# Kernel optimization log

Measured on AMD Instinct MI355X. Metric: run time of the kernel, lower is better.

Reference implementation:

```python
import jax, jax.numpy as jnp
import numpy as np

EMBED_DIM = 768
N_HEADS = 12
HEAD_DIM = EMBED_DIM // N_HEADS


def setup_inputs() -> dict:
    key = jax.random.key(0)
    ks = jax.random.split(key, 5)
    s = 1.0 / np.sqrt(EMBED_DIM)
    x = jax.random.normal(ks[0], (8, 1024, EMBED_DIM), dtype=jnp.float32)
    w_qkv = jax.random.normal(ks[1], (EMBED_DIM, 3 * EMBED_DIM), dtype=jnp.float32) * s
    b_qkv = jnp.zeros((3 * EMBED_DIM,), dtype=jnp.float32)
    w_proj = jax.random.normal(ks[2], (EMBED_DIM, EMBED_DIM), dtype=jnp.float32) * s
    b_proj = jnp.zeros((EMBED_DIM,), dtype=jnp.float32)
    return {"x": x, "w_qkv": w_qkv, "b_qkv": b_qkv, "w_proj": w_proj, "b_proj": b_proj}


def reference(x, w_qkv, b_qkv, w_proj, b_proj):
    B, S, D = x.shape
    H, Hd = N_HEADS, HEAD_DIM
    qkv = x @ w_qkv + b_qkv                      # [B,S,3D]
    qkv = qkv.reshape(B, S, 3, H, Hd).transpose(2, 0, 3, 1, 4)  # [3,B,H,S,Hd]
    q, k, v = qkv[0], qkv[1], qkv[2]
    scale = Hd ** -0.5
    attn = jnp.einsum('bhqd,bhkd->bhqk', q, k) * scale  # [B,H,S,S]
    attn = jax.nn.softmax(attn, axis=-1)
    out = jnp.einsum('bhqk,bhkd->bhqd', attn, v)        # [B,H,S,Hd]
    out = out.transpose(0, 2, 1, 3).reshape(B, S, D)
    return out @ w_proj + b_proj
```

## Files before the change

kernel.cpp:

```cpp
#include <hip/hip_runtime.h>
#include <stdint.h>

typedef unsigned short ushort_t;
typedef __bf16 bf16x8 __attribute__((ext_vector_type(8)));
typedef float floatx4 __attribute__((ext_vector_type(4)));
typedef float floatx16 __attribute__((ext_vector_type(16)));
typedef unsigned int uintx4 __attribute__((ext_vector_type(4)));

#define B_   8
#define S_   1024
#define D_   768
#define H_   12
#define M_   (B_ * S_)
#define N3_  (3 * D_)
#define QK_  1536
#define QSCALE 0.18033688f

static __device__ __forceinline__ void gl_lds16(const void* g, void* l) {
  __builtin_amdgcn_global_load_lds((const __attribute__((address_space(1))) void*)g,
                                   (__attribute__((address_space(3))) void*)l,
                                   16, 0, 0);
}

static __device__ __forceinline__ ushort_t f2bf(float f) {
  __bf16 h = (__bf16)f;
  return __builtin_bit_cast(unsigned short, h);
}

static __device__ __forceinline__ void store_out(ushort_t* p, float v) { *p = f2bf(v); }
static __device__ __forceinline__ void store_out(float* p, float v) { *p = v; }

static __device__ __forceinline__ unsigned cvt_pk_bf16(float lo, float hi) {
  unsigned d;
  asm("v_cvt_pk_bf16_f32 %0, %1, %2" : "=v"(d) : "v"(lo), "v"(hi));
  return d;
}
static __device__ __forceinline__ void plane32_swap(unsigned& a, unsigned& b) {
  asm volatile("v_permlane32_swap_b32 %0, %1" : "+v"(a), "+v"(b));
}

static __device__ __forceinline__ void transpose_tile(const float* __restrict__ W,
                                                      ushort_t* __restrict__ Wt,
                                                      int K, int N, int bx, int by,
                                                      int t) {
  __shared__ float tile[32][33];
  const int n0 = bx * 32, k0 = by * 32;
  const int tx = t & 31, ty = t >> 5;
#pragma unroll
  for (int i = 0; i < 4; ++i)
    tile[ty + i * 8][tx] = W[(size_t)(k0 + ty + i * 8) * N + n0 + tx];
  __syncthreads();
#pragma unroll
  for (int i = 0; i < 4; ++i)
    Wt[(size_t)(n0 + ty + i * 8) * K + k0 + tx] = f2bf(tile[tx][ty + i * 8]);
}

__global__ __launch_bounds__(256) void prep_kernel(const float* __restrict__ x,
                                                   ushort_t* __restrict__ xb,
                                                   const float* __restrict__ w_qkv,
                                                   ushort_t* __restrict__ wqkvt,
                                                   const float* __restrict__ w_proj,
                                                   ushort_t* __restrict__ wprojt) {
  const int gb = blockIdx.x, t = threadIdx.x;
  if (gb < 6144) {
    const int i = (gb * 256 + t) * 4;
    const float4 v = *(const float4*)(x + i);
    ushort4 o4;
    o4.x = f2bf(v.x); o4.y = f2bf(v.y); o4.z = f2bf(v.z); o4.w = f2bf(v.w);
    *(ushort4*)(xb + i) = o4;
  } else if (gb < 6144 + 1728) {
    const int lb = gb - 6144;
    transpose_tile(w_qkv, wqkvt, D_, N3_, lb % 72, lb / 72, t);
  } else {
    const int lb = gb - 6144 - 1728;
    transpose_tile(w_proj, wprojt, D_, D_, lb % 24, lb / 24, t);
  }
}

template <typename OutT, bool SPLITV>
__global__ __launch_bounds__(256) void gemm_bt_bias(const ushort_t* __restrict__ A,
                                                    const ushort_t* __restrict__ Bt,
                                                    const float* __restrict__ bias,
                                                    OutT* __restrict__ C, int CN,
                                                    ushort_t* __restrict__ vt) {
  __shared__ __align__(16) ushort_t As[128 * 32];
  __shared__ __align__(16) ushort_t Bs[128 * 32];
  const int t = threadIdx.x;
  const int wave = t >> 6, lane = t & 63;
  const int quad = lane >> 4, l15 = lane & 15;
  const int wm = wave >> 1, wn = wave & 1;
  const int m0 = blockIdx.y * 128, n0 = blockIdx.x * 128;

  const int scol  = ((lane & 3) ^ ((lane >> 3) & 3)) * 8;
  const int slotq = (quad ^ ((l15 >> 1) & 3)) * 8;

  floatx4 acc[4][4];
#pragma unroll
  for (int i = 0; i < 4; ++i)
#pragma unroll
    for (int j = 0; j < 4; ++j) acc[i][j] = (floatx4)0.0f;

  for (int k0 = 0; k0 < 768; k0 += 32) {
    if (k0) __syncthreads();
#pragma unroll
    for (int c = 0; c < 2; ++c) {
      const int i0 = c * 256 + wave * 64;
      const int i = i0 + lane;
      const int row = i >> 2;
      gl_lds16(A + (size_t)(m0 + row) * 768 + k0 + scol, As + i0 * 8);
      gl_lds16(Bt + (size_t)(n0 + row) * 768 + k0 + scol, Bs + i0 * 8);
    }
    __syncthreads();

    bf16x8 af[4], bfr[4];
#pragma unroll
    for (int mi = 0; mi < 4; ++mi)
      af[mi] = *(const bf16x8*)(As + (wm * 64 + mi * 16 + l15) * 32 + slotq);
#pragma unroll
    for (int ni = 0; ni < 4; ++ni)
      bfr[ni] = *(const bf16x8*)(Bs + (wn * 64 + ni * 16 + l15) * 32 + slotq);
#pragma unroll
    for (int mi = 0; mi < 4; ++mi)
#pragma unroll
      for (int ni = 0; ni < 4; ++ni)
        acc[mi][ni] = __builtin_amdgcn_mfma_f32_16x16x32_bf16(af[mi], bfr[ni], acc[mi][ni], 0, 0, 0);
  }

#pragma unroll
  for (int ni = 0; ni < 4; ++ni) {
    const int colb = n0 + wn * 64 + ni * 16;
    const int col = colb + l15;
    const float bb = bias[col];
    if (SPLITV && colb >= 1536) {
      const int hh = (colb - 1536) >> 6;
      const int d  = ((colb - 1536) & 63) + l15;
      const int bh = (m0 >> 10) * H_ + hh;
      ushort_t* vrow = vt + ((size_t)bh * 64 + d) * 1024 +
                       (m0 & 1023) + wm * 64 + quad * 4;
#pragma unroll
      for (int mi = 0; mi < 4; ++mi) {
        ushort4 pk;
        pk.x = f2bf(acc[mi][ni][0] + bb);
        pk.y = f2bf(acc[mi][ni][1] + bb);
        pk.z = f2bf(acc[mi][ni][2] + bb);
        pk.w = f2bf(acc[mi][ni][3] + bb);
        *(ushort4*)(vrow + mi * 16) = pk;
      }
    } else {
      const float sc = (SPLITV && colb < 768) ? QSCALE : 1.0f;
#pragma unroll
      for (int mi = 0; mi < 4; ++mi) {
#pragma unroll
        for (int r = 0; r < 4; ++r) {
          const int row = m0 + wm * 64 + mi * 16 + quad * 4 + r;
          store_out(&C[(size_t)row * CN + col], (acc[mi][ni][r] + bb) * sc);
        }
      }
    }
  }
}

__global__ __launch_bounds__(256, 3) void attn_kernel(const ushort_t* __restrict__ qk,
                                                      const ushort_t* __restrict__ vt,
                                                      ushort_t* __restrict__ o) {
  __shared__ __align__(16) ushort_t Qs[128 * 64];
  __shared__ __align__(16) ushort_t Ks[64 * 64];
  __shared__ __align__(16) ushort_t Vts[64 * 64];
  __shared__ float Ls[128];

  const int t = threadIdx.x;
  const int wave = t >> 6, lane = t & 63;
  const int l31 = lane & 31, hi = lane >> 5, l7 = lane & 7;

  const int g = blockIdx.x;
  const int xcd = g & 7, gi = g >> 3;
  const int bh = xcd * 12 + (gi >> 3);
  const int q0 = (gi & 7) * 128;
  const int h = bh % H_;
  const int bS = (bh / H_) * S_;
  const ushort_t* vbase = vt + (size_t)bh * 64 * 1024;

#pragma unroll
  for (int c = 0; c < 4; ++c) {
    const int i0 = c * 256 + wave * 64;
    const int i = i0 + lane;
    const int row = i >> 3, sg = (i & 7) ^ (row & 7);
    gl_lds16(qk + (size_t)(bS + q0 + row) * QK_ + h * 64 + sg * 8, Qs + i0 * 8);
  }
#pragma unroll
  for (int c = 0; c < 2; ++c) {
    const int i0 = c * 256 + wave * 64;
    const int i = i0 + lane;
    const int row = i >> 3, sg = (i & 7) ^ (row & 7);
    gl_lds16(qk + (size_t)(bS + row) * QK_ + 768 + h * 64 + sg * 8, Ks + i0 * 8);
    gl_lds16(vbase + (size_t)row * 1024 + sg * 8, Vts + i0 * 8);
  }
  __syncthreads();

  bf16x8 qf[4];
#pragma unroll
  for (int ks = 0; ks < 4; ++ks)
    qf[ks] = *(const bf16x8*)(Qs + (wave * 32 + l31) * 64 +
                              (((ks * 2 + hi) ^ l7) * 8));

  floatx16 oa[2];
  oa[0] = (floatx16)0.0f;
  oa[1] = (floatx16)0.0f;
  float lsum = 0.0f;

  for (int kv0 = 0; kv0 < S_; kv0 += 64) {
    if (kv0) {
      __syncthreads();
#pragma unroll
      for (int c = 0; c < 2; ++c) {
        const int i0 = c * 256 + wave * 64;
        const int i = i0 + lane;
        const int row = i >> 3, sg = (i & 7) ^ (row & 7);
        gl_lds16(qk + (size_t)(bS + kv0 + row) * QK_ + 768 + h * 64 + sg * 8,
                 Ks + i0 * 8);
        gl_lds16(vbase + (size_t)row * 1024 + kv0 + sg * 8, Vts + i0 * 8);
      }
      __syncthreads();
    }

    floatx16 sw0 = (floatx16)0.0f, sw1 = (floatx16)0.0f;
#pragma unroll
    for (int ks = 0; ks < 4; ++ks) {
      const bf16x8 kf0 = *(const bf16x8*)(Ks + (l31) * 64 + (((ks * 2 + hi) ^ l7) * 8));
      const bf16x8 kf1 = *(const bf16x8*)(Ks + (32 + l31) * 64 + (((ks * 2 + hi) ^ l7) * 8));
      sw0 = __builtin_amdgcn_mfma_f32_32x32x16_bf16(kf0, qf[ks], sw0, 0, 0, 0);
      sw1 = __builtin_amdgcn_mfma_f32_32x32x16_bf16(kf1, qf[ks], sw1, 0, 0, 0);
    }

    uintx4 pw[4];
#pragma unroll
    for (int tkv = 0; tkv < 2; ++tkv) {
      float p[16];
      float ps = 0.0f;
#pragma unroll
      for (int r = 0; r < 16; ++r) {
        p[r] = exp2f(tkv ? sw1[r] : sw0[r]);
        ps += p[r];
      }
      lsum += ps;
#pragma unroll
      for (int sub = 0; sub < 2; ++sub) {
        const int b = sub * 8;
        unsigned a0 = cvt_pk_bf16(p[b + 0], p[b + 1]);
        unsigned b0 = cvt_pk_bf16(p[b + 4], p[b + 5]);
        plane32_swap(a0, b0);
        unsigned a1 = cvt_pk_bf16(p[b + 2], p[b + 3]);
        unsigned b1 = cvt_pk_bf16(p[b + 6], p[b + 7]);
        plane32_swap(a1, b1);
        uintx4 w;
        w[0] = a0; w[1] = a1; w[2] = b0; w[3] = b1;
        pw[tkv * 2 + sub] = w;
      }
    }

#pragma unroll
    for (int dt = 0; dt < 2; ++dt)
#pragma unroll
      for (int ks4 = 0; ks4 < 4; ++ks4) {
        const bf16x8 vf = *(const bf16x8*)(Vts + (dt * 32 + l31) * 64 +
                                           (((ks4 * 2 + hi) ^ l7) * 8));
        const bf16x8 paf = __builtin_bit_cast(bf16x8, pw[ks4]);
        oa[dt] = __builtin_amdgcn_mfma_f32_32x32x16_bf16(paf, vf, oa[dt], 0, 0, 0);
      }
  }

  lsum += __shfl_xor(lsum, 32, 64);
  if (lane < 32) Ls[wave * 32 + lane] = lsum;

#pragma unroll
  for (int reg = 0; reg < 16; ++reg) {
    const int qrow = (reg & 3) + 8 * (reg >> 2) + 4 * hi;
    const float inv = 1.0f / Ls[wave * 32 + qrow];
    const int q = q0 + wave * 32 + qrow;
#pragma unroll
    for (int dt = 0; dt < 2; ++dt)
      o[(size_t)(bS + q) * D_ + h * 64 + dt * 32 + l31] = f2bf(oa[dt][reg] * inv);
  }
}

extern "C" void kernel_launch(void* const* d_in, const int* in_sizes, int n_in,
                              void* d_out, int out_size, void* d_ws, size_t ws_size,
                              hipStream_t stream) {
  const float* x      = (const float*)d_in[0];
  const float* w_qkv  = (const float*)d_in[1];
  const float* b_qkv  = (const float*)d_in[2];
  const float* w_proj = (const float*)d_in[3];
  const float* b_proj = (const float*)d_in[4];
  float* out = (float*)d_out;

  ushort_t* xb = (ushort_t*)d_out;

  ushort_t* vtb    = (ushort_t*)d_ws;
  ushort_t* wqkvt  = vtb + (size_t)96 * 64 * 1024;
  ushort_t* wprojt = wqkvt + (size_t)N3_ * D_;
  ushort_t* qkb    = wprojt + (size_t)D_ * D_;
  ushort_t* attnb  = qkb + (size_t)M_ * QK_;

  prep_kernel<<<6144 + 1728 + 576, 256, 0, stream>>>(x, xb, w_qkv, wqkvt,
                                                     w_proj, wprojt);
  gemm_bt_bias<ushort_t, true><<<dim3(N3_ / 128, M_ / 128), 256, 0, stream>>>(
      xb, wqkvt, b_qkv, qkb, QK_, vtb);
  attn_kernel<<<dim3(768), 256, 0, stream>>>(qkb, vtb, attnb);
  gemm_bt_bias<float, false><<<dim3(D_ / 128, M_ / 128), 256, 0, stream>>>(
      attnb, wprojt, b_proj, out, D_, nullptr);
}
```

Baseline: 199.1 us.

## Use 256x128 tiles with 512 threads and swizzled block order for QKV GEMM

```diff
diff --git a/kernel.cpp b/kernel.cpp
--- a/kernel.cpp
+++ b/kernel.cpp
@@ -78,6 +78,97 @@
 }
 
 template <typename OutT, bool SPLITV>
+__global__ __launch_bounds__(512, 4) void gemm_bm256(const ushort_t* __restrict__ A,
+                                                     const ushort_t* __restrict__ Bt,
+                                                     const float* __restrict__ bias,
+                                                     OutT* __restrict__ C, int CN,
+                                                     ushort_t* __restrict__ vt,
+                                                     int NBX, int CHUNK) {
+  __shared__ __align__(16) ushort_t As[256 * 32];
+  __shared__ __align__(16) ushort_t Bs[128 * 32];
+  const int t = threadIdx.x;
+  const int wave = t >> 6, lane = t & 63;
+  const int quad = lane >> 4, l15 = lane & 15;
+  const int wm = wave >> 1, wn = wave & 1;
+
+  const int g = blockIdx.x;
+  const int swz = (g & 7) * CHUNK + (g >> 3);
+  const int bx = swz % NBX, by = swz / NBX;
+  const int m0 = by * 256, n0 = bx * 128;
+
+  const int scol  = ((lane & 3) ^ ((lane >> 3) & 3)) * 8;
+  const int slotq = (quad ^ ((l15 >> 1) & 3)) * 8;
+
+  floatx4 acc[4][4];
+#pragma unroll
+  for (int i = 0; i < 4; ++i)
+#pragma unroll
+    for (int j = 0; j < 4; ++j) acc[i][j] = (floatx4)0.0f;
+
+  for (int k0 = 0; k0 < 768; k0 += 32) {
+    if (k0) __syncthreads();
+#pragma unroll
+    for (int c = 0; c < 2; ++c) {
+      const int i0 = c * 512 + wave * 64;
+      const int row = (i0 + lane) >> 2;
+      gl_lds16(A + (size_t)(m0 + row) * 768 + k0 + scol, As + i0 * 8);
+    }
+    {
+      const int i0 = wave * 64;
+      const int row = (i0 + lane) >> 2;
+      gl_lds16(Bt + (size_t)(n0 + row) * 768 + k0 + scol, Bs + i0 * 8);
+    }
+    __syncthreads();
+
+    bf16x8 af[4], bfr[4];
+#pragma unroll
+    for (int mi = 0; mi < 4; ++mi)
+      af[mi] = *(const bf16x8*)(As + (wm * 64 + mi * 16 + l15) * 32 + slotq);
+#pragma unroll
+    for (int ni = 0; ni < 4; ++ni)
+      bfr[ni] = *(const bf16x8*)(Bs + (wn * 64 + ni * 16 + l15) * 32 + slotq);
+#pragma unroll
+    for (int mi = 0; mi < 4; ++mi)
+#pragma unroll
+      for (int ni = 0; ni < 4; ++ni)
+        acc[mi][ni] = __builtin_amdgcn_mfma_f32_16x16x32_bf16(af[mi], bfr[ni], acc[mi][ni], 0, 0, 0);
+  }
+
+#pragma unroll
+  for (int ni = 0; ni < 4; ++ni) {
+    const int colb = n0 + wn * 64 + ni * 16;
+    const int col = colb + l15;
+    const float bb = bias[col];
+    if (SPLITV && colb >= 1536) {
+      const int hh = (colb - 1536) >> 6;
+      const int d  = ((colb - 1536) & 63) + l15;
+      const int bh = (m0 >> 10) * H_ + hh;
+      ushort_t* vrow = vt + ((size_t)bh * 64 + d) * 1024 +
+                       (m0 & 1023) + wm * 64 + quad * 4;
+#pragma unroll
+      for (int mi = 0; mi < 4; ++mi) {
+        ushort4 pk;
+        pk.x = f2bf(acc[mi][ni][0] + bb);
+        pk.y = f2bf(acc[mi][ni][1] + bb);
+        pk.z = f2bf(acc[mi][ni][2] + bb);
+        pk.w = f2bf(acc[mi][ni][3] + bb);
+        *(ushort4*)(vrow + mi * 16) = pk;
+      }
+    } else {
+      const float sc = (SPLITV && colb < 768) ? QSCALE : 1.0f;
+#pragma unroll
+      for (int mi = 0; mi < 4; ++mi) {
+#pragma unroll
+        for (int r = 0; r < 4; ++r) {
+          const int row = m0 + wm * 64 + mi * 16 + quad * 4 + r;
+          store_out(&C[(size_t)row * CN + col], (acc[mi][ni][r] + bb) * sc);
+        }
+      }
+    }
+  }
+}
+
+template <typename OutT, bool SPLITV>
 __global__ __launch_bounds__(256) void gemm_bt_bias(const ushort_t* __restrict__ A,
                                                     const ushort_t* __restrict__ Bt,
                                                     const float* __restrict__ bias,
@@ -303,8 +394,8 @@
 
   prep_kernel<<<6144 + 1728 + 576, 256, 0, stream>>>(x, xb, w_qkv, wqkvt,
                                                      w_proj, wprojt);
-  gemm_bt_bias<ushort_t, true><<<dim3(N3_ / 128, M_ / 128), 256, 0, stream>>>(
-      xb, wqkvt, b_qkv, qkb, QK_, vtb);
+  gemm_bm256<ushort_t, true><<<576, 512, 0, stream>>>(xb, wqkvt, b_qkv, qkb,
+                                                      QK_, vtb, 18, 72);
   attn_kernel<<<dim3(768), 256, 0, stream>>>(qkb, vtb, attnb);
   gemm_bt_bias<float, false><<<dim3(D_ / 128, M_ / 128), 256, 0, stream>>>(
       attnb, wprojt, b_proj, out, D_, nullptr);
```

After: 203.6 us. 2.3% more time.
